# Performance work log

Measured on AMD Instinct MI355X. Metric: run time of the kernel, lower is better.

## Reference

```python
import jax, jax.numpy as jnp
import numpy as np


def setup_inputs() -> dict:
    key = jax.random.key(0)
    k1, k2 = jax.random.split(key)
    B, N, D = 4, 2048, 1024
    x = jax.random.normal(k1, (B, N, D), dtype=jnp.float32)
    # torch nn.Linear weight shape [out_features, in_features] = [3D, D]
    w_qkv = jax.random.normal(k2, (3 * D, D), dtype=jnp.float32) * (D ** -0.5)
    return {"x": x, "w_qkv": w_qkv}


def reference(x, w_qkv):
    D = x.shape[-1]
    scale = D ** -0.5
    qkv = jnp.einsum('bnd,ed->bne', x, w_qkv)  # [B, N, 3D]
    q, k, v = jnp.split(qkv, 3, axis=-1)
    scores = jnp.einsum('bnd,bmd->bnm', q, k) * scale  # [B, N, N]
    attn = jax.nn.softmax(scores, axis=-1)
    return jnp.einsum('bnm,bmd->bnd', attn, v)
```

## Files before the change

kernel.cpp:

```cpp
#include <hip/hip_runtime.h>
#include <hip/hip_bf16.h>


typedef __bf16 bf16x8 __attribute__((ext_vector_type(8)));
typedef float f32x4 __attribute__((ext_vector_type(4)));

__device__ __forceinline__ void gload_lds16(const __hip_bfloat16* g, __hip_bfloat16* l) {
  __builtin_amdgcn_global_load_lds(
      (const __attribute__((address_space(1))) void*)g,
      (__attribute__((address_space(3))) void*)l, 16, 0, 0);
}

__device__ __forceinline__ void store_out(float* p, float v) { *p = v; }
__device__ __forceinline__ void store_out(__hip_bfloat16* p, float v) { *p = __float2bfloat16(v); }

__global__ __launch_bounds__(256)
void cast_f32_bf16(const float* __restrict__ in, __hip_bfloat16* __restrict__ out, int n4) {
  for (int i = blockIdx.x * blockDim.x + threadIdx.x; i < n4; i += gridDim.x * blockDim.x) {
    float4 v = ((const float4*)in)[i];
    __hip_bfloat16 b0 = __float2bfloat16(v.x), b1 = __float2bfloat16(v.y),
                   b2 = __float2bfloat16(v.z), b3 = __float2bfloat16(v.w);
    ushort4 o;
    o.x = *(unsigned short*)&b0; o.y = *(unsigned short*)&b1;
    o.z = *(unsigned short*)&b2; o.w = *(unsigned short*)&b3;
    ((ushort4*)out)[i] = o;
  }
}

template <typename OutT>
__global__ __launch_bounds__(256)
void gemm_bt(const __hip_bfloat16* __restrict__ A, int lda, long sA,
             const __hip_bfloat16* __restrict__ B, int ldb, long sB,
             OutT* __restrict__ C, int ldc, long sC,
             int K, float cscale) {
  constexpr int BK = 64;
  __shared__ __hip_bfloat16 As[128 * BK];
  __shared__ __hip_bfloat16 Bs[128 * BK];
  const int tid = threadIdx.x, lane = tid & 63, wid = tid >> 6;
  const int wr = wid >> 1, wc = wid & 1;
  A += (long)blockIdx.z * sA; B += (long)blockIdx.z * sB; C += (long)blockIdx.z * sC;
  const long bm = (long)blockIdx.x * 128, bn = (long)blockIdx.y * 128;
  const int lrow = lane & 15, lk8 = lane >> 4;
  f32x4 acc[4][4] = {};

  for (int k0 = 0; k0 < K; k0 += BK) {
#pragma unroll
    for (int i = 0; i < 4; ++i) {
      int p = i * 256 + tid;
      int row = p >> 3, g = p & 7;
      gload_lds16(A + (bm + row) * (long)lda + k0 + g * 8, &As[(i * 256 + (wid << 6)) * 8]);
    }
#pragma unroll
    for (int i = 0; i < 4; ++i) {
      int p = i * 256 + tid;
      int row = p >> 3, g = p & 7;
      gload_lds16(B + (bn + row) * (long)ldb + k0 + g * 8, &Bs[(i * 256 + (wid << 6)) * 8]);
    }
    __syncthreads();
#pragma unroll
    for (int kk = 0; kk < 2; ++kk) {
      bf16x8 af[4], bfr[4];
#pragma unroll
      for (int m = 0; m < 4; ++m)
        af[m] = *(const bf16x8*)&As[(wr * 64 + m * 16 + lrow) * BK + kk * 32 + lk8 * 8];
#pragma unroll
      for (int n = 0; n < 4; ++n)
        bfr[n] = *(const bf16x8*)&Bs[(wc * 64 + n * 16 + lrow) * BK + kk * 32 + lk8 * 8];
#pragma unroll
      for (int m = 0; m < 4; ++m)
#pragma unroll
        for (int n = 0; n < 4; ++n)
          acc[m][n] = __builtin_amdgcn_mfma_f32_16x16x32_bf16(af[m], bfr[n], acc[m][n], 0, 0, 0);
    }
    __syncthreads();
  }

  const int r0 = (lane >> 4) * 4;
#pragma unroll
  for (int m = 0; m < 4; ++m)
#pragma unroll
    for (int n = 0; n < 4; ++n) {
      long col = bn + wc * 64 + n * 16 + lrow;
      long row = bm + wr * 64 + m * 16 + r0;
#pragma unroll
      for (int j = 0; j < 4; ++j)
        store_out(&C[(row + j) * (long)ldc + col], acc[m][n][j] * cscale);
    }
}

__global__ __launch_bounds__(256)
void transpose_v(const __hip_bfloat16* __restrict__ qkv, __hip_bfloat16* __restrict__ Vt) {
  __shared__ __hip_bfloat16 tile[32][33];
  const int b = blockIdx.z;
  const __hip_bfloat16* V = qkv + (size_t)b * 2048 * 3072 + 2048;
  __hip_bfloat16* vt = Vt + (size_t)b * 1024 * 2048;
  const int tx = threadIdx.x & 31, ty = threadIdx.x >> 5;
  const int m0 = blockIdx.x * 32, d0 = blockIdx.y * 32;
#pragma unroll
  for (int i = 0; i < 32; i += 8)
    tile[ty + i][tx] = V[(size_t)(m0 + ty + i) * 3072 + d0 + tx];
  __syncthreads();
#pragma unroll
  for (int i = 0; i < 32; i += 8)
    vt[(size_t)(d0 + ty + i) * 2048 + m0 + tx] = tile[tx][ty + i];
}

__global__ __launch_bounds__(256)
void softmax_rows(float* __restrict__ S) {
  float* row = S + (size_t)blockIdx.x * 2048;
  const int t = threadIdx.x, lane = t & 63, wid = t >> 6;
  float4 v0 = ((const float4*)row)[t];
  float4 v1 = ((const float4*)row)[256 + t];
  float vals[8] = {v0.x, v0.y, v0.z, v0.w, v1.x, v1.y, v1.z, v1.w};
  float m = vals[0];
#pragma unroll
  for (int i = 1; i < 8; ++i) m = fmaxf(m, vals[i]);
#pragma unroll
  for (int o = 32; o; o >>= 1) m = fmaxf(m, __shfl_xor(m, o));
  __shared__ float red[4];
  if (lane == 0) red[wid] = m;
  __syncthreads();
  m = fmaxf(fmaxf(red[0], red[1]), fmaxf(red[2], red[3]));
  __syncthreads();
  float p[8], s = 0.f;
#pragma unroll
  for (int i = 0; i < 8; ++i) { p[i] = __expf(vals[i] - m); s += p[i]; }
#pragma unroll
  for (int o = 32; o; o >>= 1) s += __shfl_xor(s, o);
  if (lane == 0) red[wid] = s;
  __syncthreads();
  s = red[0] + red[1] + red[2] + red[3];
  const float inv = 1.0f / s;
  __hip_bfloat16 b[8];
#pragma unroll
  for (int i = 0; i < 8; ++i) b[i] = __float2bfloat16(p[i] * inv);
  ushort4 o0, o1;
  o0.x = *(unsigned short*)&b[0]; o0.y = *(unsigned short*)&b[1];
  o0.z = *(unsigned short*)&b[2]; o0.w = *(unsigned short*)&b[3];
  o1.x = *(unsigned short*)&b[4]; o1.y = *(unsigned short*)&b[5];
  o1.z = *(unsigned short*)&b[6]; o1.w = *(unsigned short*)&b[7];
  unsigned short* prow = (unsigned short*)row;
  ((ushort4*)prow)[t] = o0;
  ((ushort4*)prow)[256 + t] = o1;
}

extern "C" void kernel_launch(void* const* d_in, const int* in_sizes, int n_in,
                              void* d_out, int out_size, void* d_ws, size_t ws_size,
                              hipStream_t stream) {
  const float* x = (const float*)d_in[0];
  const float* w = (const float*)d_in[1];
  float* out = (float*)d_out;
  char* ws = (char*)d_ws;

  __hip_bfloat16* xb  = (__hip_bfloat16*)ws;
  __hip_bfloat16* wb  = (__hip_bfloat16*)(ws + 16777216);
  float*          S   = (float*)ws;
  __hip_bfloat16* qkv = (__hip_bfloat16*)(ws + 67108864);
  __hip_bfloat16* Vt  = (__hip_bfloat16*)(ws + 117440512);

  cast_f32_bf16<<<1024, 256, 0, stream>>>(x, xb, (4 * 2048 * 1024) / 4);
  cast_f32_bf16<<<512, 256, 0, stream>>>(w, wb, (3072 * 1024) / 4);

  gemm_bt<__hip_bfloat16><<<dim3(64, 24, 1), 256, 0, stream>>>(
      xb, 1024, 0L, wb, 1024, 0L, qkv, 3072, 0L, 1024, 1.0f);

  transpose_v<<<dim3(64, 32, 4), 256, 0, stream>>>(qkv, Vt);

  gemm_bt<float><<<dim3(16, 16, 4), 256, 0, stream>>>(
      qkv, 3072, (long)2048 * 3072, qkv + 1024, 3072, (long)2048 * 3072,
      S, 2048, (long)2048 * 2048, 1024, 0.03125f);

  softmax_rows<<<8192, 256, 0, stream>>>(S);

  gemm_bt<float><<<dim3(16, 8, 4), 256, 0, stream>>>(
      (const __hip_bfloat16*)S, 4096, (long)2048 * 4096,
      Vt, 2048, (long)1024 * 2048,
      out, 1024, (long)2048 * 1024, 2048, 1.0f);
}
```

Before: 293.2 us.

## Replace GEMM with 256x256 double-buffered, swizzled, phase-pipelined MFMA kernel

Replaces the 128x128 single-buffered GEMM with a 256x256-tile kernel using 8 waves, 128KB of dynamic LDS double buffering, and XOR-swizzled LDS layout. Global-to-LDS prefetch of the next K tile is interleaved with four compute phases, using explicit waitcnt, barriers and s_setprio. The aim is to hide memory latency, cut LDS bank conflicts and raise arithmetic intensity. The risks are lower occupancy with fewer blocks for the small grids (e.g. 128 blocks for the PV GEMM) and fragile hand-tuned wait counts.

```diff
diff --git a/kernel.cpp b/kernel.cpp
--- a/kernel.cpp
+++ b/kernel.cpp
@@ -4,12 +4,6 @@
 
 typedef __bf16 bf16x8 __attribute__((ext_vector_type(8)));
 typedef float f32x4 __attribute__((ext_vector_type(4)));
-
-__device__ __forceinline__ void gload_lds16(const __hip_bfloat16* g, __hip_bfloat16* l) {
-  __builtin_amdgcn_global_load_lds(
-      (const __attribute__((address_space(1))) void*)g,
-      (__attribute__((address_space(3))) void*)l, 16, 0, 0);
-}
 
 __device__ __forceinline__ void store_out(float* p, float v) { *p = v; }
 __device__ __forceinline__ void store_out(__hip_bfloat16* p, float v) { *p = __float2bfloat16(v); }
@@ -27,64 +21,109 @@
   }
 }
 
+
+#define PHASE(P, CB, PF, K0N)                                                          \
+  {                                                                                    \
+    bf16x8 a00 = frag(CB, 0, wm * 128 + P * 32 +  0, 0);                               \
+    bf16x8 a01 = frag(CB, 0, wm * 128 + P * 32 +  0, 1);                               \
+    bf16x8 a10 = frag(CB, 0, wm * 128 + P * 32 + 16, 0);                               \
+    bf16x8 a11 = frag(CB, 0, wm * 128 + P * 32 + 16, 1);                               \
+    if (P == 0) {                                                                      \
+      _Pragma("unroll") for (int j = 0; j < 4; ++j) {                                  \
+        bfr[j][0] = frag(CB, 1, wn * 64 + j * 16, 0);                                  \
+        bfr[j][1] = frag(CB, 1, wn * 64 + j * 16, 1);                                  \
+      }                                                                                \
+    }                                                                                  \
+    if (PF) {                                                                          \
+      if (P == 0) { stage(CB ^ 1, 0,   0, K0N); stage(CB ^ 1, 0, 128, K0N); }          \
+      if (P == 1) { stage(CB ^ 1, 1,   0, K0N); stage(CB ^ 1, 1,  64, K0N); }          \
+      if (P == 2) { stage(CB ^ 1, 1, 128, K0N); stage(CB ^ 1, 1, 192, K0N); }          \
+      if (P == 3) { stage(CB ^ 1, 0,  64, K0N); stage(CB ^ 1, 0, 192, K0N); }          \
+    }                                                                                  \
+    if (P == 0) asm volatile("s_waitcnt lgkmcnt(8)" ::: "memory");                     \
+    if (P == 1) {                                                                      \
+      if (PF) asm volatile("s_waitcnt vmcnt(4)" ::: "memory");                         \
+      else    asm volatile("s_waitcnt vmcnt(0)" ::: "memory");                         \
+    }                                                                                  \
+    if (P == 3) { if (PF) asm volatile("s_waitcnt vmcnt(2)" ::: "memory"); }           \
+    __builtin_amdgcn_s_barrier();                                                      \
+    asm volatile("s_waitcnt lgkmcnt(0)" ::: "memory");                                 \
+    __builtin_amdgcn_sched_barrier(0);                                                 \
+    __builtin_amdgcn_s_setprio(1);                                                     \
+    _Pragma("unroll") for (int j = 0; j < 4; ++j) {                                    \
+      acc[P * 2 + 0][j] = __builtin_amdgcn_mfma_f32_16x16x32_bf16(a00, bfr[j][0], acc[P * 2 + 0][j], 0, 0, 0); \
+      acc[P * 2 + 0][j] = __builtin_amdgcn_mfma_f32_16x16x32_bf16(a01, bfr[j][1], acc[P * 2 + 0][j], 0, 0, 0); \
+      acc[P * 2 + 1][j] = __builtin_amdgcn_mfma_f32_16x16x32_bf16(a10, bfr[j][0], acc[P * 2 + 1][j], 0, 0, 0); \
+      acc[P * 2 + 1][j] = __builtin_amdgcn_mfma_f32_16x16x32_bf16(a11, bfr[j][1], acc[P * 2 + 1][j], 0, 0, 0); \
+    }                                                                                  \
+    __builtin_amdgcn_s_setprio(0);                                                     \
+    __builtin_amdgcn_s_barrier();                                                      \
+  }
+
 template <typename OutT>
-__global__ __launch_bounds__(256)
-void gemm_bt(const __hip_bfloat16* __restrict__ A, int lda, long sA,
+__global__ __launch_bounds__(512, 2)
+void gemm256(const __hip_bfloat16* __restrict__ A, int lda, long sA,
              const __hip_bfloat16* __restrict__ B, int ldb, long sB,
              OutT* __restrict__ C, int ldc, long sC,
              int K, float cscale) {
-  constexpr int BK = 64;
-  __shared__ __hip_bfloat16 As[128 * BK];
-  __shared__ __hip_bfloat16 Bs[128 * BK];
+  extern __shared__ char smem[];
   const int tid = threadIdx.x, lane = tid & 63, wid = tid >> 6;
-  const int wr = wid >> 1, wc = wid & 1;
+  const int wm = wid >> 2, wn = wid & 3;
   A += (long)blockIdx.z * sA; B += (long)blockIdx.z * sB; C += (long)blockIdx.z * sC;
-  const long bm = (long)blockIdx.x * 128, bn = (long)blockIdx.y * 128;
-  const int lrow = lane & 15, lk8 = lane >> 4;
-  f32x4 acc[4][4] = {};
-
-  for (int k0 = 0; k0 < K; k0 += BK) {
-#pragma unroll
-    for (int i = 0; i < 4; ++i) {
-      int p = i * 256 + tid;
-      int row = p >> 3, g = p & 7;
-      gload_lds16(A + (bm + row) * (long)lda + k0 + g * 8, &As[(i * 256 + (wid << 6)) * 8]);
+  const long bm = (long)blockIdx.x * 256, bn = (long)blockIdx.y * 256;
+  const int laneOff = (lane & 15) * 64 + (((lane >> 4) * 16) ^ ((lane & 8) ? 32 : 0));
+  const int sRowA = (wid >> 1) * 16 + (lane >> 2);
+  const int sKs   = wid & 1;
+  const int sCol  = ((lane & 3) * 8) ^ ((lane & 32) ? 16 : 0);
+  const int nt = K >> 6;
+
+  auto stage = [&](int cbuf, int reg , int row0, int k0) {
+    const __hip_bfloat16* g =
+        reg ? (B + (bn + row0 + sRowA) * (long)ldb + k0 + sKs * 32 + sCol)
+            : (A + (bm + row0 + sRowA) * (long)lda + k0 + sKs * 32 + sCol);
+    char* dst = smem + cbuf * 65536 + reg * 32768 + ((row0 >> 4) * 2 + wid) * 1024;
+    __builtin_amdgcn_global_load_lds((const __attribute__((address_space(1))) void*)g,
+                                     (__attribute__((address_space(3))) void*)dst, 16, 0, 0);
+  };
+  auto frag = [&](int cbuf, int reg, int R, int ks) -> bf16x8 {
+    return *(const bf16x8*)(smem + cbuf * 65536 + reg * 32768 +
+                            ((R >> 4) * 2 + ks) * 1024 + laneOff);
+  };
+
+  f32x4 acc[8][4] = {};
+  bf16x8 bfr[4][2];
+
+  stage(0, 0,   0, 0); stage(0, 0, 128, 0);
+  stage(0, 1,   0, 0); stage(0, 1,  64, 0);
+  stage(0, 1, 128, 0); stage(0, 1, 192, 0);
+  stage(0, 0,  64, 0); stage(0, 0, 192, 0);
+  asm volatile("s_waitcnt vmcnt(2)" ::: "memory");
+  __builtin_amdgcn_s_barrier();
+
+  for (int t = 0; t < nt; t += 2) {
+    {
+      const int k0n = (t + 1) << 6;
+      PHASE(0, 0, true, k0n) PHASE(1, 0, true, k0n)
+      PHASE(2, 0, true, k0n) PHASE(3, 0, true, k0n)
     }
-#pragma unroll
-    for (int i = 0; i < 4; ++i) {
-      int p = i * 256 + tid;
-      int row = p >> 3, g = p & 7;
-      gload_lds16(B + (bn + row) * (long)ldb + k0 + g * 8, &Bs[(i * 256 + (wid << 6)) * 8]);
+    {
+      const bool pf = (t + 2) < nt;
+      const int k0n = (t + 2) << 6;
+      PHASE(0, 1, pf, k0n) PHASE(1, 1, pf, k0n)
+      PHASE(2, 1, pf, k0n) PHASE(3, 1, pf, k0n)
     }
-    __syncthreads();
-#pragma unroll
-    for (int kk = 0; kk < 2; ++kk) {
-      bf16x8 af[4], bfr[4];
-#pragma unroll
-      for (int m = 0; m < 4; ++m)
-        af[m] = *(const bf16x8*)&As[(wr * 64 + m * 16 + lrow) * BK + kk * 32 + lk8 * 8];
-#pragma unroll
-      for (int n = 0; n < 4; ++n)
-        bfr[n] = *(const bf16x8*)&Bs[(wc * 64 + n * 16 + lrow) * BK + kk * 32 + lk8 * 8];
-#pragma unroll
-      for (int m = 0; m < 4; ++m)
-#pragma unroll
-        for (int n = 0; n < 4; ++n)
-          acc[m][n] = __builtin_amdgcn_mfma_f32_16x16x32_bf16(af[m], bfr[n], acc[m][n], 0, 0, 0);
-    }
-    __syncthreads();
   }
 
-  const int r0 = (lane >> 4) * 4;
-#pragma unroll
-  for (int m = 0; m < 4; ++m)
-#pragma unroll
-    for (int n = 0; n < 4; ++n) {
-      long col = bn + wc * 64 + n * 16 + lrow;
-      long row = bm + wr * 64 + m * 16 + r0;
-#pragma unroll
-      for (int j = 0; j < 4; ++j)
-        store_out(&C[(row + j) * (long)ldc + col], acc[m][n][j] * cscale);
+  const int r0 = (lane >> 4) * 4, cn = lane & 15;
+#pragma unroll
+  for (int rf = 0; rf < 8; ++rf)
+#pragma unroll
+    for (int j = 0; j < 4; ++j) {
+      long row = bm + wm * 128 + rf * 16 + r0;
+      long col = bn + wn * 64 + j * 16 + cn;
+#pragma unroll
+      for (int jj = 0; jj < 4; ++jj)
+        store_out(&C[(row + jj) * (long)ldc + col], acc[rf][j][jj] * cscale);
     }
 }
 
@@ -161,18 +200,18 @@
   cast_f32_bf16<<<1024, 256, 0, stream>>>(x, xb, (4 * 2048 * 1024) / 4);
   cast_f32_bf16<<<512, 256, 0, stream>>>(w, wb, (3072 * 1024) / 4);
 
-  gemm_bt<__hip_bfloat16><<<dim3(64, 24, 1), 256, 0, stream>>>(
+  gemm256<__hip_bfloat16><<<dim3(32, 12, 1), 512, 131072, stream>>>(
       xb, 1024, 0L, wb, 1024, 0L, qkv, 3072, 0L, 1024, 1.0f);
 
   transpose_v<<<dim3(64, 32, 4), 256, 0, stream>>>(qkv, Vt);
 
-  gemm_bt<float><<<dim3(16, 16, 4), 256, 0, stream>>>(
+  gemm256<float><<<dim3(8, 8, 4), 512, 131072, stream>>>(
       qkv, 3072, (long)2048 * 3072, qkv + 1024, 3072, (long)2048 * 3072,
       S, 2048, (long)2048 * 2048, 1024, 0.03125f);
 
   softmax_rows<<<8192, 256, 0, stream>>>(S);
 
-  gemm_bt<float><<<dim3(16, 8, 4), 256, 0, stream>>>(
+  gemm256<float><<<dim3(8, 4, 4), 512, 131072, stream>>>(
       (const __hip_bfloat16*)S, 4096, (long)2048 * 4096,
       Vt, 2048, (long)1024 * 2048,
       out, 1024, (long)2048 * 1024, 2048, 1.0f);
```

Measured after the change: 267.9 us. 1.09x faster.
